# Kernel tuning notes

Hardware: AMD Instinct MI355X
Metric: run time of the kernel (lower is better)

The kernel has to match this reference:

```python
import jax, jax.numpy as jnp
import numpy as np

B = 4096
D0, D1 = 256, 64


def setup_inputs() -> dict:
    key = jax.random.key(0)
    k0, k1, k2, k3 = jax.random.split(key, 4)
    return {
        "s0": jax.random.normal(k0, (B, D0), dtype=jnp.float32),
        "s1": jax.random.normal(k1, (B, D1), dtype=jnp.float32),
        "t0": jax.random.normal(k2, (B, D0), dtype=jnp.float32),
        "t1": jax.random.normal(k3, (B, D1), dtype=jnp.float32),
    }


def _gaussian_kernel(source, target):
    # feats: [2B, D]
    feats = jnp.concatenate([source, target], axis=0)
    n = feats.shape[0]
    # pairwise squared distances [2B, 2B] via the Gram-matrix identity
    # (same math as ((x - y) ** 2).sum(-1), avoids the [N, N, D] intermediate)
    sq = jnp.sum(feats * feats, axis=-1)
    dist = sq[:, None] + sq[None, :] - 2.0 * (feats @ feats.T)
    # median-heuristic bandwidth with num_kernels=1: gamma = (n^2 - n) / sum(dist)
    gamma = (n * n - n) / jnp.sum(jax.lax.stop_gradient(dist))
    return jnp.exp(-dist * gamma)


def reference(s0, s1, t0, t1):
    # joint kernel: elementwise product of per-stream Gaussian kernels
    k = _gaussian_kernel(s0, t0) * _gaussian_kernel(s1, t1)
    b = s0.shape[0]
    s2s = k[:b, :b]
    t2t = k[b:, b:]
    s2t = k[:b, b:]
    return jnp.mean(s2s + t2t - 2.0 * s2t)
```

## Files before the change

### kernel.cpp

```cpp
#include <hip/hip_runtime.h>
#include <hip/hip_fp8.h>

#define B_ROWS 4096
#define NTOT   8192
#define D0     256
#define D1     64
#define KDIM   320
#define NSB    128
#define NTILE  64
#define NTRI   2080

typedef __attribute__((ext_vector_type(4))) float f32x4;
typedef __attribute__((ext_vector_type(2))) long long2v;

#define OFF_GAM   0
#define OFF_PQ0   32
#define OFF_PQ1   544
#define OFF_P0    1056
#define OFF_P1    132128
#define OFF_R     164896
#define OFF_BSUM  197664
#define OFF_PHI   214304

__device__ __forceinline__ void load_lds16(const void* g, void* l) {
    __builtin_amdgcn_global_load_lds(
        (const __attribute__((address_space(1))) void*)g,
        (__attribute__((address_space(3))) void*)l, 16, 0, 0);
}

__global__ __launch_bounds__(256) void k_stats(
    const float* __restrict__ s0, const float* __restrict__ s1,
    const float* __restrict__ t0, const float* __restrict__ t1,
    float* __restrict__ part0, float* __restrict__ part1,
    float* __restrict__ pq0, float* __restrict__ pq1) {
    __shared__ float sh0[4][256];
    __shared__ float sh1[4][64];
    __shared__ float shq[4][2];
    int t = threadIdx.x, wv = t >> 6, lane = t & 63;
    int rb = blockIdx.x * 64;
    int c4 = lane * 4;
    int rr = wv;

    f32x4 cs = {0.f, 0.f, 0.f, 0.f};
    float q0 = 0.f;
    #pragma unroll 4
    for (int k = 0; k < 16; ++k) {
        int row = rb + rr + k * 4;
        const float* b0 = (row < B_ROWS) ? s0 + (size_t)row * D0 : t0 + (size_t)(row - B_ROWS) * D0;
        f32x4 v = *(const f32x4*)(b0 + c4);
        cs.x += v.x; cs.y += v.y; cs.z += v.z; cs.w += v.w;
        q0 += v.x * v.x + v.y * v.y + v.z * v.z + v.w * v.w;
    }
    *(f32x4*)&sh0[rr][c4] = cs;

    float cs1 = 0.f, q1 = 0.f;
    #pragma unroll 4
    for (int k = 0; k < 16; ++k) {
        int row = rb + rr + k * 4;
        const float* b1 = (row < B_ROWS) ? s1 + (size_t)row * D1 : t1 + (size_t)(row - B_ROWS) * D1;
        float v = b1[lane];
        cs1 += v; q1 += v * v;
    }
    sh1[rr][lane] = cs1;

    #pragma unroll
    for (int o = 32; o; o >>= 1) { q0 += __shfl_xor(q0, o, 64); q1 += __shfl_xor(q1, o, 64); }
    if (lane == 0) { shq[wv][0] = q0; shq[wv][1] = q1; }
    __syncthreads();

    part0[blockIdx.x * D0 + t] = sh0[0][t] + sh0[1][t] + sh0[2][t] + sh0[3][t];
    if (t < D1) part1[blockIdx.x * D1 + t] = sh1[0][t] + sh1[1][t] + sh1[2][t] + sh1[3][t];
    if (t == 0) {
        pq0[blockIdx.x] = shq[0][0] + shq[1][0] + shq[2][0] + shq[3][0];
        pq1[blockIdx.x] = shq[0][1] + shq[1][1] + shq[2][1] + shq[3][1];
    }
}

__global__ __launch_bounds__(256) void k_gamma(
    const float* __restrict__ pq0, const float* __restrict__ pq1,
    const float* __restrict__ part0, const float* __restrict__ part1,
    float* __restrict__ gam) {
    __shared__ double sh[4][4];
    int t = threadIdx.x, wv = t >> 6, lane = t & 63;

    double a0 = 0.0, a1 = 0.0;
    if (t < NSB) { a0 = (double)pq0[t]; a1 = (double)pq1[t]; }

    double F0t = 0.0;
    for (int b = 0; b < NSB; ++b) F0t += (double)part0[b * D0 + t];
    double nf0 = F0t * F0t;

    double nf1 = 0.0;
    if (t < D1) {
        double F1t = 0.0;
        for (int b = 0; b < NSB; ++b) F1t += (double)part1[b * D1 + t];
        nf1 = F1t * F1t;
    }

    #pragma unroll
    for (int o = 32; o; o >>= 1) {
        a0  += __shfl_xor(a0, o, 64);
        a1  += __shfl_xor(a1, o, 64);
        nf0 += __shfl_xor(nf0, o, 64);
        nf1 += __shfl_xor(nf1, o, 64);
    }
    if (lane == 0) { sh[wv][0] = a0; sh[wv][1] = a1; sh[wv][2] = nf0; sh[wv][3] = nf1; }
    __syncthreads();
    if (t == 0) {
        double b0 = 0, b1 = 0, b2 = 0, b3 = 0;
        for (int w = 0; w < 4; ++w) { b0 += sh[w][0]; b1 += sh[w][1]; b2 += sh[w][2]; b3 += sh[w][3]; }
        double n = (double)NTOT;
        double g0 = (n * n - n) / (2.0 * n * b0 - 2.0 * b2);
        double g1 = (n * n - n) / (2.0 * n * b1 - 2.0 * b3);
        gam[0] = (float)g0; gam[1] = (float)g1;
        gam[2] = (float)sqrt(g0); gam[3] = (float)sqrt(g1);
    }
}

__global__ __launch_bounds__(256) void k_pack(
    const float* __restrict__ s0, const float* __restrict__ s1,
    const float* __restrict__ t0, const float* __restrict__ t1,
    const float* __restrict__ gam, unsigned char* __restrict__ phi,
    float* __restrict__ rvec) {
    int wv = threadIdx.x >> 6, lane = threadIdx.x & 63;
    int row = blockIdx.x * 4 + wv;
    float sg0 = gam[2], sg1 = gam[3];
    const float* b0 = (row < B_ROWS) ? s0 + (size_t)row * D0 : t0 + (size_t)(row - B_ROWS) * D0;
    const float* b1 = (row < B_ROWS) ? s1 + (size_t)row * D1 : t1 + (size_t)(row - B_ROWS) * D1;
    unsigned char* pr = phi + (size_t)row * KDIM;
    f32x4 v = *(const f32x4*)(b0 + lane * 4);
    __hip_fp8_e4m3 q0(v.x * sg0), q1(v.y * sg0), q2(v.z * sg0), q3(v.w * sg0);
    unsigned int word = (unsigned int)q0.__x | ((unsigned int)q1.__x << 8) |
                        ((unsigned int)q2.__x << 16) | ((unsigned int)q3.__x << 24);
    int doff0 = ((lane >> 4) << 6) + (((lane >> 1) & 3) << 4) +
                (((lane >> 3) & 1) << 3) + ((lane & 1) << 2);
    *(unsigned int*)(pr + doff0) = word;
    float f0 = (float)q0, f1 = (float)q1, f2 = (float)q2, f3 = (float)q3;
    float p = f0 * f0 + f1 * f1 + f2 * f2 + f3 * f3;
    __hip_fp8_e4m3 qd(b1[lane] * sg1);
    int doff1 = 256 + (((lane >> 3) & 3) << 4) + (((lane >> 5) & 1) << 3) + (lane & 7);
    pr[doff1] = qd.__x;
    float fd = (float)qd;
    p += fd * fd;
    #pragma unroll
    for (int o = 32; o; o >>= 1) p += __shfl_xor(p, o, 64);
    if (lane == 0) rvec[row] = p;
}

__global__ __launch_bounds__(256, 3) void k_mmd(
    const unsigned char* __restrict__ phi, const float* __restrict__ rvec,
    double* __restrict__ blocksum) {
    int tb = blockIdx.x;
    int I = (int)((129.0f - sqrtf(16641.0f - 8.0f * (float)tb)) * 0.5f);
    while ((129 * I - I * I) / 2 > tb) --I;
    while ((129 * (I + 1) - (I + 1) * (I + 1)) / 2 <= tb) ++I;
    int J = I + (tb - (129 * I - I * I) / 2);

    __shared__ unsigned char As[24576];
    __shared__ unsigned char Bs[24576];
    __shared__ float rIl[128], rJl[128];
    __shared__ float wsum[4];

    int tid = threadIdx.x, wv = tid >> 6, lane = tid & 63;
    int wr = wv >> 1, wc = wv & 1;
    int rgrp = lane >> 4, rlow = lane & 15;
    const int rowA = I * 128, rowB = J * 128;

    if (tid < 128) rIl[tid] = rvec[rowA + tid];
    else           rJl[tid - 128] = rvec[rowB + (tid - 128)];

    f32x4 acc_[4][4] = {};

    #define STAGE(tbase, nt)                                                    \
        _Pragma("unroll")                                                       \
        for (int it = 0; it < (nt) * 2; ++it) {                                 \
            int idx = it * 256 + tid;                                           \
            int tt = idx >> 9, rs = idx & 511;                                  \
            int row = rs >> 2, slot = rs & 3;                                   \
            int rg = slot ^ ((row >> 1) & 3);                                   \
            size_t gcol = ((tbase) + tt) * 64 + rg * 16;                        \
            load_lds16(phi + (size_t)(rowA + row) * KDIM + gcol,                \
                       As + it * 4096 + wv * 1024);                             \
            load_lds16(phi + (size_t)(rowB + row) * KDIM + gcol,                \
                       Bs + it * 4096 + wv * 1024);                             \
        }

    #define COMPUTE(kkbase, nt)                                                 \
        _Pragma("unroll")                                                       \
        for (int tt = 0; tt < (nt); ++tt) {                                     \
            long2v af[4], bf[4];                                                \
            _Pragma("unroll")                                                   \
            for (int m = 0; m < 4; ++m) {                                       \
                int row = wr * 64 + m * 16 + rlow;                              \
                int slot = rgrp ^ ((row >> 1) & 3);                             \
                af[m] = *(const long2v*)&As[tt * 8192 + row * 64 + slot * 16];  \
            }                                                                   \
            _Pragma("unroll")                                                   \
            for (int n = 0; n < 4; ++n) {                                       \
                int col = wc * 64 + n * 16 + rlow;                              \
                int slot = rgrp ^ ((col >> 1) & 3);                             \
                bf[n] = *(const long2v*)&Bs[tt * 8192 + col * 64 + slot * 16];  \
            }                                                                   \
            _Pragma("unroll")                                                   \
            for (int m = 0; m < 4; ++m)                                         \
                _Pragma("unroll")                                               \
                for (int n = 0; n < 4; ++n) {                                   \
                    acc_[m][n] = __builtin_amdgcn_mfma_f32_16x16x32_fp8_fp8(    \
                        af[m][0], bf[n][0], acc_[m][n], 0, 0, 0);               \
                    acc_[m][n] = __builtin_amdgcn_mfma_f32_16x16x32_fp8_fp8(    \
                        af[m][1], bf[n][1], acc_[m][n], 0, 0, 0);               \
                }                                                               \
        }

    STAGE(0, 3);
    __syncthreads();
    COMPUTE(0, 3);
    __syncthreads();
    STAGE(3, 2);
    __syncthreads();
    COMPUTE(6, 2);

    float psum = 0.f;
    #pragma unroll
    for (int m = 0; m < 4; ++m) {
        float ri[4];
        #pragma unroll
        for (int j = 0; j < 4; ++j) ri[j] = rIl[wr * 64 + m * 16 + rgrp * 4 + j];
        #pragma unroll
        for (int n = 0; n < 4; ++n) {
            float rj = rJl[wc * 64 + n * 16 + rlow];
            f32x4 a = acc_[m][n];
            psum += __expf(2.f * a.x - ri[0] - rj);
            psum += __expf(2.f * a.y - ri[1] - rj);
            psum += __expf(2.f * a.z - ri[2] - rj);
            psum += __expf(2.f * a.w - ri[3] - rj);
        }
    }
    #pragma unroll
    for (int o = 32; o; o >>= 1) psum += __shfl_xor(psum, o, 64);
    if (lane == 0) wsum[wv] = psum;
    __syncthreads();
    if (tid == 0) {
        float bs = wsum[0] + wsum[1] + wsum[2] + wsum[3];
        double sgn = ((I < 32) == (J < 32)) ? 1.0 : -1.0;
        double fac = (I == J) ? 1.0 : 2.0;
        blocksum[tb] = sgn * fac * (double)bs;
    }
}

__global__ __launch_bounds__(256) void k_final(
    const double* __restrict__ blocksum, float* __restrict__ out) {
    __shared__ double sh[4];
    int t = threadIdx.x, wv = t >> 6, lane = t & 63;
    double s = 0.0;
    for (int i = t; i < NTRI; i += 256) s += blocksum[i];
    #pragma unroll
    for (int o = 32; o; o >>= 1) s += __shfl_xor(s, o, 64);
    if (lane == 0) sh[wv] = s;
    __syncthreads();
    if (t == 0) {
        double tot = sh[0] + sh[1] + sh[2] + sh[3];
        out[0] = (float)(tot / ((double)B_ROWS * (double)B_ROWS));
    }
}

extern "C" void kernel_launch(void* const* d_in, const int* in_sizes, int n_in,
                              void* d_out, int out_size, void* d_ws, size_t ws_size,
                              hipStream_t stream) {
    const float* s0 = (const float*)d_in[0];
    const float* s1 = (const float*)d_in[1];
    const float* t0 = (const float*)d_in[2];
    const float* t1 = (const float*)d_in[3];
    char* ws = (char*)d_ws;
    float*  gam  = (float*)(ws + OFF_GAM);
    float*  pq0  = (float*)(ws + OFF_PQ0);
    float*  pq1  = (float*)(ws + OFF_PQ1);
    float*  p0   = (float*)(ws + OFF_P0);
    float*  p1   = (float*)(ws + OFF_P1);
    float*  rvec = (float*)(ws + OFF_R);
    double* bsum = (double*)(ws + OFF_BSUM);
    unsigned char* phi = (unsigned char*)(ws + OFF_PHI);

    k_stats<<<NSB, 256, 0, stream>>>(s0, s1, t0, t1, p0, p1, pq0, pq1);
    k_gamma<<<1, 256, 0, stream>>>(pq0, pq1, p0, p1, gam);
    k_pack<<<2048, 256, 0, stream>>>(s0, s1, t0, t1, gam, phi, rvec);
    k_mmd<<<NTRI, 256, 0, stream>>>(phi, rvec, bsum);
    k_final<<<1, 256, 0, stream>>>(bsum, (float*)d_out);
}
```

Measured before the change: 49.73 us.

## Pipeline K-chunk LDS loads with per-chunk vmcnt waits in fp8 MFMA tile

Replaces the two-phase stage/compute schedule with a three-slot ring of 64-wide K chunks. Later chunks' global-to-LDS loads are issued while earlier chunks are computed, and partial s_waitcnt vmcnt counts let each chunk start as soon as its own data lands. It also raises wave priority around the MFMA block with s_setprio. The goal is to hide global load latency behind matrix math. The risk is subtle hazards from manual waitcnt and barrier ordering, plus ring-slot reuse.

```diff
diff --git a/kernel.cpp b/kernel.cpp
--- a/kernel.cpp
+++ b/kernel.cpp
@@ -27,6 +27,11 @@
         (const __attribute__((address_space(1))) void*)g,
         (__attribute__((address_space(3))) void*)l, 16, 0, 0);
 }
+
+#define VMCNT(n) asm volatile("s_waitcnt vmcnt(" #n ")" ::: "memory")
+#define BAR()    do { asm volatile("" ::: "memory");            \
+                      __builtin_amdgcn_s_barrier();             \
+                      asm volatile("" ::: "memory"); } while (0)
 
 __global__ __launch_bounds__(256) void k_stats(
     const float* __restrict__ s0, const float* __restrict__ s1,
@@ -168,39 +173,39 @@
 
     if (tid < 128) rIl[tid] = rvec[rowA + tid];
     else           rJl[tid - 128] = rvec[rowB + (tid - 128)];
+    asm volatile("s_waitcnt lgkmcnt(0)" ::: "memory");
 
     f32x4 acc_[4][4] = {};
 
-    #define STAGE(tbase, nt)                                                    \
+    #define STAGE_CHUNK(c)                                                      \
         _Pragma("unroll")                                                       \
-        for (int it = 0; it < (nt) * 2; ++it) {                                 \
+        for (int it = 0; it < 2; ++it) {                                        \
             int idx = it * 256 + tid;                                           \
-            int tt = idx >> 9, rs = idx & 511;                                  \
-            int row = rs >> 2, slot = rs & 3;                                   \
+            int row = idx >> 2, slot = idx & 3;                                 \
             int rg = slot ^ ((row >> 1) & 3);                                   \
-            size_t gcol = ((tbase) + tt) * 64 + rg * 16;                        \
+            size_t gcol = (size_t)(c) * 64 + rg * 16;                           \
             load_lds16(phi + (size_t)(rowA + row) * KDIM + gcol,                \
-                       As + it * 4096 + wv * 1024);                             \
+                       As + ((c) % 3) * 8192 + it * 4096 + wv * 1024);          \
             load_lds16(phi + (size_t)(rowB + row) * KDIM + gcol,                \
-                       Bs + it * 4096 + wv * 1024);                             \
+                       Bs + ((c) % 3) * 8192 + it * 4096 + wv * 1024);          \
         }
 
-    #define COMPUTE(kkbase, nt)                                                 \
-        _Pragma("unroll")                                                       \
-        for (int tt = 0; tt < (nt); ++tt) {                                     \
+    #define COMPUTE_SLOT(s)                                                     \
+        {                                                                       \
             long2v af[4], bf[4];                                                \
             _Pragma("unroll")                                                   \
             for (int m = 0; m < 4; ++m) {                                       \
                 int row = wr * 64 + m * 16 + rlow;                              \
-                int slot = rgrp ^ ((row >> 1) & 3);                             \
-                af[m] = *(const long2v*)&As[tt * 8192 + row * 64 + slot * 16];  \
+                int sl = rgrp ^ ((row >> 1) & 3);                               \
+                af[m] = *(const long2v*)&As[(s) * 8192 + row * 64 + sl * 16];   \
             }                                                                   \
             _Pragma("unroll")                                                   \
             for (int n = 0; n < 4; ++n) {                                       \
                 int col = wc * 64 + n * 16 + rlow;                              \
-                int slot = rgrp ^ ((col >> 1) & 3);                             \
-                bf[n] = *(const long2v*)&Bs[tt * 8192 + col * 64 + slot * 16];  \
+                int sl = rgrp ^ ((col >> 1) & 3);                               \
+                bf[n] = *(const long2v*)&Bs[(s) * 8192 + col * 64 + sl * 16];   \
             }                                                                   \
+            __builtin_amdgcn_s_setprio(1);                                      \
             _Pragma("unroll")                                                   \
             for (int m = 0; m < 4; ++m)                                         \
                 _Pragma("unroll")                                               \
@@ -210,15 +215,27 @@
                     acc_[m][n] = __builtin_amdgcn_mfma_f32_16x16x32_fp8_fp8(    \
                         af[m][1], bf[n][1], acc_[m][n], 0, 0, 0);               \
                 }                                                               \
+            __builtin_amdgcn_s_setprio(0);                                      \
         }
 
-    STAGE(0, 3);
-    __syncthreads();
-    COMPUTE(0, 3);
-    __syncthreads();
-    STAGE(3, 2);
-    __syncthreads();
-    COMPUTE(6, 2);
+    STAGE_CHUNK(0);
+    STAGE_CHUNK(1);
+    STAGE_CHUNK(2);
+
+    VMCNT(8); BAR();
+    COMPUTE_SLOT(0);
+    BAR();
+    STAGE_CHUNK(3);
+    VMCNT(8); BAR();
+    COMPUTE_SLOT(1);
+    BAR();
+    STAGE_CHUNK(4);
+    VMCNT(8); BAR();
+    COMPUTE_SLOT(2);
+    VMCNT(4); BAR();
+    COMPUTE_SLOT(0);
+    VMCNT(0); BAR();
+    COMPUTE_SLOT(1);
 
     float psum = 0.f;
     #pragma unroll
```

Measured after the change: 51.41 us. 3.4% more time.

## Fuse stats, gamma and pack kernels via grid-wide atomic barrier; raise MFMA priority

Applied to the files above, without the earlier changes.

Merges the three preprocessing kernels (column stats, gamma reduction, fp8 packing) into one persistent-style kernel of 256 blocks. The blocks synchronise through an atomic counter spin barrier, then each block redundantly reduces all partials to compute gamma and packs its own 32 rows. This removes two kernel launches and the tiny single-block gamma kernel from the critical path. The cost is a memset, a spin barrier that relies on all 256 blocks being co-resident, and redundant reduction work in every block. It also wraps the MFMA loop in s_setprio to favour the math waves.

```diff
diff --git a/kernel.cpp b/kernel.cpp
--- a/kernel.cpp
+++ b/kernel.cpp
@@ -6,21 +6,21 @@
 #define D0     256
 #define D1     64
 #define KDIM   320
-#define NSB    128
+#define PB     256
 #define NTILE  64
 #define NTRI   2080
 
 typedef __attribute__((ext_vector_type(4))) float f32x4;
 typedef __attribute__((ext_vector_type(2))) long long2v;
 
-#define OFF_GAM   0
-#define OFF_PQ0   32
-#define OFF_PQ1   544
-#define OFF_P0    1056
-#define OFF_P1    132128
-#define OFF_R     164896
-#define OFF_BSUM  197664
-#define OFF_PHI   214304
+#define OFF_CNT   0
+#define OFF_PQ0   16
+#define OFF_PQ1   1040
+#define OFF_P0    2064
+#define OFF_P1    264208
+#define OFF_R     329744
+#define OFF_BSUM  362512
+#define OFF_PHI   379152
 
 __device__ __forceinline__ void load_lds16(const void* g, void* l) {
     __builtin_amdgcn_global_load_lds(
@@ -28,123 +28,117 @@
         (__attribute__((address_space(3))) void*)l, 16, 0, 0);
 }
 
-__global__ __launch_bounds__(256) void k_stats(
+__global__ __launch_bounds__(256) void k_prep(
     const float* __restrict__ s0, const float* __restrict__ s1,
     const float* __restrict__ t0, const float* __restrict__ t1,
     float* __restrict__ part0, float* __restrict__ part1,
-    float* __restrict__ pq0, float* __restrict__ pq1) {
-    __shared__ float sh0[4][256];
+    float* __restrict__ pq0, float* __restrict__ pq1,
+    unsigned char* __restrict__ phi, float* __restrict__ rvec,
+    int* __restrict__ cnt) {
     __shared__ float sh1[4][64];
     __shared__ float shq[4][2];
+    __shared__ double shd[4][4];
+    __shared__ float shg[2];
     int t = threadIdx.x, wv = t >> 6, lane = t & 63;
-    int rb = blockIdx.x * 64;
-    int c4 = lane * 4;
-    int rr = wv;
-
-    f32x4 cs = {0.f, 0.f, 0.f, 0.f};
-    float q0 = 0.f;
+    int b = blockIdx.x;
+    int rb = b * 32;
+
+    float cs0 = 0.f, q0 = 0.f;
     #pragma unroll 4
-    for (int k = 0; k < 16; ++k) {
-        int row = rb + rr + k * 4;
-        const float* b0 = (row < B_ROWS) ? s0 + (size_t)row * D0 : t0 + (size_t)(row - B_ROWS) * D0;
-        f32x4 v = *(const f32x4*)(b0 + c4);
-        cs.x += v.x; cs.y += v.y; cs.z += v.z; cs.w += v.w;
-        q0 += v.x * v.x + v.y * v.y + v.z * v.z + v.w * v.w;
-    }
-    *(f32x4*)&sh0[rr][c4] = cs;
+    for (int r = 0; r < 32; ++r) {
+        int row = rb + r;
+        const float* p = (row < B_ROWS) ? s0 + (size_t)row * D0
+                                        : t0 + (size_t)(row - B_ROWS) * D0;
+        float v = p[t];
+        cs0 += v; q0 += v * v;
+    }
+    part0[b * D0 + t] = cs0;
 
     float cs1 = 0.f, q1 = 0.f;
     #pragma unroll 4
-    for (int k = 0; k < 16; ++k) {
-        int row = rb + rr + k * 4;
-        const float* b1 = (row < B_ROWS) ? s1 + (size_t)row * D1 : t1 + (size_t)(row - B_ROWS) * D1;
-        float v = b1[lane];
+    for (int r = 0; r < 8; ++r) {
+        int row = rb + wv * 8 + r;
+        const float* p = (row < B_ROWS) ? s1 + (size_t)row * D1
+                                        : t1 + (size_t)(row - B_ROWS) * D1;
+        float v = p[lane];
         cs1 += v; q1 += v * v;
     }
-    sh1[rr][lane] = cs1;
-
+    sh1[wv][lane] = cs1;
     #pragma unroll
     for (int o = 32; o; o >>= 1) { q0 += __shfl_xor(q0, o, 64); q1 += __shfl_xor(q1, o, 64); }
     if (lane == 0) { shq[wv][0] = q0; shq[wv][1] = q1; }
     __syncthreads();
-
-    part0[blockIdx.x * D0 + t] = sh0[0][t] + sh0[1][t] + sh0[2][t] + sh0[3][t];
-    if (t < D1) part1[blockIdx.x * D1 + t] = sh1[0][t] + sh1[1][t] + sh1[2][t] + sh1[3][t];
-    if (t == 0) {
-        pq0[blockIdx.x] = shq[0][0] + shq[1][0] + shq[2][0] + shq[3][0];
-        pq1[blockIdx.x] = shq[0][1] + shq[1][1] + shq[2][1] + shq[3][1];
-    }
-}
-
-__global__ __launch_bounds__(256) void k_gamma(
-    const float* __restrict__ pq0, const float* __restrict__ pq1,
-    const float* __restrict__ part0, const float* __restrict__ part1,
-    float* __restrict__ gam) {
-    __shared__ double sh[4][4];
-    int t = threadIdx.x, wv = t >> 6, lane = t & 63;
-
-    double a0 = 0.0, a1 = 0.0;
-    if (t < NSB) { a0 = (double)pq0[t]; a1 = (double)pq1[t]; }
+    if (t < D1) part1[b * D1 + t] = sh1[0][t] + sh1[1][t] + sh1[2][t] + sh1[3][t];
+    if (t == 0) {
+        pq0[b] = shq[0][0] + shq[1][0] + shq[2][0] + shq[3][0];
+        pq1[b] = shq[0][1] + shq[1][1] + shq[2][1] + shq[3][1];
+    }
+    __syncthreads();
+    if (t == 0) {
+        __threadfence();
+        __hip_atomic_fetch_add(cnt, 1, __ATOMIC_RELEASE, __HIP_MEMORY_SCOPE_AGENT);
+        while (__hip_atomic_load(cnt, __ATOMIC_ACQUIRE, __HIP_MEMORY_SCOPE_AGENT) < PB)
+            __builtin_amdgcn_s_sleep(8);
+    }
+    __syncthreads();
+    __threadfence();
 
     double F0t = 0.0;
-    for (int b = 0; b < NSB; ++b) F0t += (double)part0[b * D0 + t];
+    for (int bb = 0; bb < PB; ++bb) F0t += (double)part0[bb * D0 + t];
     double nf0 = F0t * F0t;
-
+    double ssq0 = (double)pq0[t];
+    double ssq1 = (double)pq1[t];
     double nf1 = 0.0;
     if (t < D1) {
         double F1t = 0.0;
-        for (int b = 0; b < NSB; ++b) F1t += (double)part1[b * D1 + t];
+        for (int bb = 0; bb < PB; ++bb) F1t += (double)part1[bb * D1 + t];
         nf1 = F1t * F1t;
     }
-
     #pragma unroll
     for (int o = 32; o; o >>= 1) {
-        a0  += __shfl_xor(a0, o, 64);
-        a1  += __shfl_xor(a1, o, 64);
-        nf0 += __shfl_xor(nf0, o, 64);
-        nf1 += __shfl_xor(nf1, o, 64);
-    }
-    if (lane == 0) { sh[wv][0] = a0; sh[wv][1] = a1; sh[wv][2] = nf0; sh[wv][3] = nf1; }
+        ssq0 += __shfl_xor(ssq0, o, 64);
+        ssq1 += __shfl_xor(ssq1, o, 64);
+        nf0  += __shfl_xor(nf0, o, 64);
+        nf1  += __shfl_xor(nf1, o, 64);
+    }
+    if (lane == 0) { shd[wv][0] = ssq0; shd[wv][1] = ssq1; shd[wv][2] = nf0; shd[wv][3] = nf1; }
     __syncthreads();
     if (t == 0) {
         double b0 = 0, b1 = 0, b2 = 0, b3 = 0;
-        for (int w = 0; w < 4; ++w) { b0 += sh[w][0]; b1 += sh[w][1]; b2 += sh[w][2]; b3 += sh[w][3]; }
+        for (int w = 0; w < 4; ++w) { b0 += shd[w][0]; b1 += shd[w][1]; b2 += shd[w][2]; b3 += shd[w][3]; }
         double n = (double)NTOT;
         double g0 = (n * n - n) / (2.0 * n * b0 - 2.0 * b2);
         double g1 = (n * n - n) / (2.0 * n * b1 - 2.0 * b3);
-        gam[0] = (float)g0; gam[1] = (float)g1;
-        gam[2] = (float)sqrt(g0); gam[3] = (float)sqrt(g1);
-    }
-}
-
-__global__ __launch_bounds__(256) void k_pack(
-    const float* __restrict__ s0, const float* __restrict__ s1,
-    const float* __restrict__ t0, const float* __restrict__ t1,
-    const float* __restrict__ gam, unsigned char* __restrict__ phi,
-    float* __restrict__ rvec) {
-    int wv = threadIdx.x >> 6, lane = threadIdx.x & 63;
-    int row = blockIdx.x * 4 + wv;
-    float sg0 = gam[2], sg1 = gam[3];
-    const float* b0 = (row < B_ROWS) ? s0 + (size_t)row * D0 : t0 + (size_t)(row - B_ROWS) * D0;
-    const float* b1 = (row < B_ROWS) ? s1 + (size_t)row * D1 : t1 + (size_t)(row - B_ROWS) * D1;
-    unsigned char* pr = phi + (size_t)row * KDIM;
-    f32x4 v = *(const f32x4*)(b0 + lane * 4);
-    __hip_fp8_e4m3 q0(v.x * sg0), q1(v.y * sg0), q2(v.z * sg0), q3(v.w * sg0);
-    unsigned int word = (unsigned int)q0.__x | ((unsigned int)q1.__x << 8) |
-                        ((unsigned int)q2.__x << 16) | ((unsigned int)q3.__x << 24);
-    int doff0 = ((lane >> 4) << 6) + (((lane >> 1) & 3) << 4) +
-                (((lane >> 3) & 1) << 3) + ((lane & 1) << 2);
-    *(unsigned int*)(pr + doff0) = word;
-    float f0 = (float)q0, f1 = (float)q1, f2 = (float)q2, f3 = (float)q3;
-    float p = f0 * f0 + f1 * f1 + f2 * f2 + f3 * f3;
-    __hip_fp8_e4m3 qd(b1[lane] * sg1);
-    int doff1 = 256 + (((lane >> 3) & 3) << 4) + (((lane >> 5) & 1) << 3) + (lane & 7);
-    pr[doff1] = qd.__x;
-    float fd = (float)qd;
-    p += fd * fd;
-    #pragma unroll
-    for (int o = 32; o; o >>= 1) p += __shfl_xor(p, o, 64);
-    if (lane == 0) rvec[row] = p;
+        shg[0] = (float)sqrt(g0); shg[1] = (float)sqrt(g1);
+    }
+    __syncthreads();
+    float sg0 = shg[0], sg1 = shg[1];
+
+    for (int r = 0; r < 8; ++r) {
+        int row = rb + wv * 8 + r;
+        const float* b0p = (row < B_ROWS) ? s0 + (size_t)row * D0
+                                          : t0 + (size_t)(row - B_ROWS) * D0;
+        const float* b1p = (row < B_ROWS) ? s1 + (size_t)row * D1
+                                          : t1 + (size_t)(row - B_ROWS) * D1;
+        unsigned char* pr = phi + (size_t)row * KDIM;
+        f32x4 v = *(const f32x4*)(b0p + lane * 4);
+        __hip_fp8_e4m3 a0(v.x * sg0), a1(v.y * sg0), a2(v.z * sg0), a3(v.w * sg0);
+        unsigned int word = (unsigned int)a0.__x | ((unsigned int)a1.__x << 8) |
+                            ((unsigned int)a2.__x << 16) | ((unsigned int)a3.__x << 24);
+        int doff0 = ((lane >> 4) << 6) + (((lane >> 1) & 3) << 4) +
+                    (((lane >> 3) & 1) << 3) + ((lane & 1) << 2);
+        *(unsigned int*)(pr + doff0) = word;
+        float f0 = (float)a0, f1 = (float)a1, f2 = (float)a2, f3 = (float)a3;
+        float p = f0 * f0 + f1 * f1 + f2 * f2 + f3 * f3;
+        __hip_fp8_e4m3 qd(b1p[lane] * sg1);
+        int doff1 = 256 + (((lane >> 3) & 3) << 4) + (((lane >> 5) & 1) << 3) + (lane & 7);
+        pr[doff1] = qd.__x;
+        float fd = (float)qd;
+        p += fd * fd;
+        #pragma unroll
+        for (int o = 32; o; o >>= 1) p += __shfl_xor(p, o, 64);
+        if (lane == 0) rvec[row] = p;
+    }
 }
 
 __global__ __launch_bounds__(256, 3) void k_mmd(
@@ -192,15 +186,16 @@
             _Pragma("unroll")                                                   \
             for (int m = 0; m < 4; ++m) {                                       \
                 int row = wr * 64 + m * 16 + rlow;                              \
-                int slot = rgrp ^ ((row >> 1) & 3);                             \
-                af[m] = *(const long2v*)&As[tt * 8192 + row * 64 + slot * 16];  \
+                int sl = rgrp ^ ((row >> 1) & 3);                               \
+                af[m] = *(const long2v*)&As[tt * 8192 + row * 64 + sl * 16];    \
             }                                                                   \
             _Pragma("unroll")                                                   \
             for (int n = 0; n < 4; ++n) {                                       \
                 int col = wc * 64 + n * 16 + rlow;                              \
-                int slot = rgrp ^ ((col >> 1) & 3);                             \
-                bf[n] = *(const long2v*)&Bs[tt * 8192 + col * 64 + slot * 16];  \
+                int sl = rgrp ^ ((col >> 1) & 3);                               \
+                bf[n] = *(const long2v*)&Bs[tt * 8192 + col * 64 + sl * 16];    \
             }                                                                   \
+            __builtin_amdgcn_s_setprio(1);                                      \
             _Pragma("unroll")                                                   \
             for (int m = 0; m < 4; ++m)                                         \
                 _Pragma("unroll")                                               \
@@ -210,6 +205,7 @@
                     acc_[m][n] = __builtin_amdgcn_mfma_f32_16x16x32_fp8_fp8(    \
                         af[m][1], bf[n][1], acc_[m][n], 0, 0, 0);               \
                 }                                                               \
+            __builtin_amdgcn_s_setprio(0);                                      \
         }
 
     STAGE(0, 3);
@@ -272,7 +268,7 @@
     const float* t0 = (const float*)d_in[2];
     const float* t1 = (const float*)d_in[3];
     char* ws = (char*)d_ws;
-    float*  gam  = (float*)(ws + OFF_GAM);
+    int*    cnt  = (int*)(ws + OFF_CNT);
     float*  pq0  = (float*)(ws + OFF_PQ0);
     float*  pq1  = (float*)(ws + OFF_PQ1);
     float*  p0   = (float*)(ws + OFF_P0);
@@ -281,9 +277,8 @@
     double* bsum = (double*)(ws + OFF_BSUM);
     unsigned char* phi = (unsigned char*)(ws + OFF_PHI);
 
-    k_stats<<<NSB, 256, 0, stream>>>(s0, s1, t0, t1, p0, p1, pq0, pq1);
-    k_gamma<<<1, 256, 0, stream>>>(pq0, pq1, p0, p1, gam);
-    k_pack<<<2048, 256, 0, stream>>>(s0, s1, t0, t1, gam, phi, rvec);
+    hipMemsetAsync(cnt, 0, 16, stream);
+    k_prep<<<PB, 256, 0, stream>>>(s0, s1, t0, t1, p0, p1, pq0, pq1, phi, rvec, cnt);
     k_mmd<<<NTRI, 256, 0, stream>>>(phi, rvec, bsum);
     k_final<<<1, 256, 0, stream>>>(bsum, (float*)d_out);
 }
```

Measured after the change: 92.37 us. +85.8%, slower.

## Stage full K in LDS at once, remap block order, drop rvec LDS staging

Applied to the files above, without the earlier changes.

The MMD kernel now loads all five K-chunks of both 128-row tiles into 80KB of LDS in one pass with a single barrier, replacing the earlier two-phase stage/compute split. Block indices are permuted across eight groups, which likely spreads work over XCDs or cache, and MFMA sections are wrapped in s_setprio. The rvec values are read directly from global memory instead of being staged in LDS, and the wave-sum scratch reuses As. The larger LDS footprint lowers the occupancy target from 3 to 2 blocks per CU, giving less latency hiding in exchange for fewer barriers.

```diff
diff --git a/kernel.cpp b/kernel.cpp
--- a/kernel.cpp
+++ b/kernel.cpp
@@ -147,101 +147,93 @@
     if (lane == 0) rvec[row] = p;
 }
 
-__global__ __launch_bounds__(256, 3) void k_mmd(
+__global__ __launch_bounds__(256, 2) void k_mmd(
     const unsigned char* __restrict__ phi, const float* __restrict__ rvec,
     double* __restrict__ blocksum) {
-    int tb = blockIdx.x;
+    int tb = (blockIdx.x & 7) * (NTRI / 8) + (blockIdx.x >> 3);
     int I = (int)((129.0f - sqrtf(16641.0f - 8.0f * (float)tb)) * 0.5f);
     while ((129 * I - I * I) / 2 > tb) --I;
     while ((129 * (I + 1) - (I + 1) * (I + 1)) / 2 <= tb) ++I;
     int J = I + (tb - (129 * I - I * I) / 2);
 
-    __shared__ unsigned char As[24576];
-    __shared__ unsigned char Bs[24576];
-    __shared__ float rIl[128], rJl[128];
-    __shared__ float wsum[4];
+    __shared__ unsigned char As[40960];
+    __shared__ unsigned char Bs[40960];
 
     int tid = threadIdx.x, wv = tid >> 6, lane = tid & 63;
     int wr = wv >> 1, wc = wv & 1;
     int rgrp = lane >> 4, rlow = lane & 15;
+    int wvb = wv * 1024;
     const int rowA = I * 128, rowB = J * 128;
 
-    if (tid < 128) rIl[tid] = rvec[rowA + tid];
-    else           rJl[tid - 128] = rvec[rowB + (tid - 128)];
-
     f32x4 acc_[4][4] = {};
 
-    #define STAGE(tbase, nt)                                                    \
-        _Pragma("unroll")                                                       \
-        for (int it = 0; it < (nt) * 2; ++it) {                                 \
-            int idx = it * 256 + tid;                                           \
-            int tt = idx >> 9, rs = idx & 511;                                  \
-            int row = rs >> 2, slot = rs & 3;                                   \
-            int rg = slot ^ ((row >> 1) & 3);                                   \
-            size_t gcol = ((tbase) + tt) * 64 + rg * 16;                        \
-            load_lds16(phi + (size_t)(rowA + row) * KDIM + gcol,                \
-                       As + it * 4096 + wv * 1024);                             \
-            load_lds16(phi + (size_t)(rowB + row) * KDIM + gcol,                \
-                       Bs + it * 4096 + wv * 1024);                             \
-        }
-
-    #define COMPUTE(kkbase, nt)                                                 \
-        _Pragma("unroll")                                                       \
-        for (int tt = 0; tt < (nt); ++tt) {                                     \
-            long2v af[4], bf[4];                                                \
-            _Pragma("unroll")                                                   \
-            for (int m = 0; m < 4; ++m) {                                       \
-                int row = wr * 64 + m * 16 + rlow;                              \
-                int slot = rgrp ^ ((row >> 1) & 3);                             \
-                af[m] = *(const long2v*)&As[tt * 8192 + row * 64 + slot * 16];  \
-            }                                                                   \
-            _Pragma("unroll")                                                   \
-            for (int n = 0; n < 4; ++n) {                                       \
-                int col = wc * 64 + n * 16 + rlow;                              \
-                int slot = rgrp ^ ((col >> 1) & 3);                             \
-                bf[n] = *(const long2v*)&Bs[tt * 8192 + col * 64 + slot * 16];  \
-            }                                                                   \
-            _Pragma("unroll")                                                   \
-            for (int m = 0; m < 4; ++m)                                         \
-                _Pragma("unroll")                                               \
-                for (int n = 0; n < 4; ++n) {                                   \
-                    acc_[m][n] = __builtin_amdgcn_mfma_f32_16x16x32_fp8_fp8(    \
-                        af[m][0], bf[n][0], acc_[m][n], 0, 0, 0);               \
-                    acc_[m][n] = __builtin_amdgcn_mfma_f32_16x16x32_fp8_fp8(    \
-                        af[m][1], bf[n][1], acc_[m][n], 0, 0, 0);               \
-                }                                                               \
-        }
-
-    STAGE(0, 3);
-    __syncthreads();
-    COMPUTE(0, 3);
-    __syncthreads();
-    STAGE(3, 2);
-    __syncthreads();
-    COMPUTE(6, 2);
+    #pragma unroll
+    for (int c = 0; c < 5; ++c) {
+        #pragma unroll
+        for (int it = 0; it < 2; ++it) {
+            int u = it * 256 + tid;
+            int row = u >> 2, sl = u & 3;
+            int rg = sl ^ ((row >> 1) & 3);
+            size_t gcol = (size_t)c * 64 + rg * 16;
+            load_lds16(phi + (size_t)(rowA + row) * KDIM + gcol,
+                       As + c * 8192 + it * 4096 + wvb);
+            load_lds16(phi + (size_t)(rowB + row) * KDIM + gcol,
+                       Bs + c * 8192 + it * 4096 + wvb);
+        }
+    }
+    __syncthreads();
+
+    #pragma unroll
+    for (int tt = 0; tt < 5; ++tt) {
+        long2v af[4], bf[4];
+        #pragma unroll
+        for (int m = 0; m < 4; ++m) {
+            int row = wr * 64 + m * 16 + rlow;
+            int sl = rgrp ^ ((row >> 1) & 3);
+            af[m] = *(const long2v*)&As[tt * 8192 + row * 64 + sl * 16];
+        }
+        #pragma unroll
+        for (int n = 0; n < 4; ++n) {
+            int col = wc * 64 + n * 16 + rlow;
+            int sl = rgrp ^ ((col >> 1) & 3);
+            bf[n] = *(const long2v*)&Bs[tt * 8192 + col * 64 + sl * 16];
+        }
+        __builtin_amdgcn_s_setprio(1);
+        #pragma unroll
+        for (int m = 0; m < 4; ++m)
+            #pragma unroll
+            for (int n = 0; n < 4; ++n) {
+                acc_[m][n] = __builtin_amdgcn_mfma_f32_16x16x32_fp8_fp8(
+                    af[m][0], bf[n][0], acc_[m][n], 0, 0, 0);
+                acc_[m][n] = __builtin_amdgcn_mfma_f32_16x16x32_fp8_fp8(
+                    af[m][1], bf[n][1], acc_[m][n], 0, 0, 0);
+            }
+        __builtin_amdgcn_s_setprio(0);
+    }
 
     float psum = 0.f;
     #pragma unroll
     for (int m = 0; m < 4; ++m) {
-        float ri[4];
-        #pragma unroll
-        for (int j = 0; j < 4; ++j) ri[j] = rIl[wr * 64 + m * 16 + rgrp * 4 + j];
+        f32x4 ri = *(const f32x4*)&rvec[rowA + wr * 64 + m * 16 + rgrp * 4];
         #pragma unroll
         for (int n = 0; n < 4; ++n) {
-            float rj = rJl[wc * 64 + n * 16 + rlow];
+            float rj = rvec[rowB + wc * 64 + n * 16 + rlow];
             f32x4 a = acc_[m][n];
-            psum += __expf(2.f * a.x - ri[0] - rj);
-            psum += __expf(2.f * a.y - ri[1] - rj);
-            psum += __expf(2.f * a.z - ri[2] - rj);
-            psum += __expf(2.f * a.w - ri[3] - rj);
+            psum += __expf(2.f * a.x - ri.x - rj);
+            psum += __expf(2.f * a.y - ri.y - rj);
+            psum += __expf(2.f * a.z - ri.z - rj);
+            psum += __expf(2.f * a.w - ri.w - rj);
         }
     }
     #pragma unroll
     for (int o = 32; o; o >>= 1) psum += __shfl_xor(psum, o, 64);
-    if (lane == 0) wsum[wv] = psum;
+
+    __syncthreads();
+    float* ws = (float*)As;
+    if (lane == 0) ws[wv] = psum;
     __syncthreads();
     if (tid == 0) {
-        float bs = wsum[0] + wsum[1] + wsum[2] + wsum[3];
+        float bs = ws[0] + ws[1] + ws[2] + ws[3];
         double sgn = ((I < 32) == (J < 32)) ? 1.0 : -1.0;
         double fac = (I == J) ? 1.0 : 2.0;
         blocksum[tb] = sgn * fac * (double)bs;
```

After: 55.83 us. 1.12x slower.
